# Kernel optimization log

Hardware: AMD Instinct MI355X
Metric: run time of the kernel (lower is better)

## Reference

```python
import jax, jax.numpy as jnp
import numpy as np

NUM_HEADS = 12
EPS = 1e-5


def _pool_norm(t, w, g, b, thw, stride):
    # t: [B, heads, 1+L, hd]. Depthwise Conv3d pooling on non-cls tokens, then LayerNorm(hd).
    B, Hn, _, hd = t.shape
    cls, body = t[:, :, :1], t[:, :, 1:]
    T, Hs, Ws = thw
    x = body.reshape(B * Hn, T, Hs, Ws, hd).transpose(0, 4, 1, 2, 3)  # [B*heads, hd, T, H, W]
    pad = [(w.shape[2] // 2,) * 2, (w.shape[3] // 2,) * 2, (w.shape[4] // 2,) * 2]
    y = jax.lax.conv_general_dilated(x, w, window_strides=stride, padding=pad,
                                     feature_group_count=hd,
                                     dimension_numbers=('NCDHW', 'OIDHW', 'NCDHW'))
    Tp, Hp, Wp = y.shape[2], y.shape[3], y.shape[4]
    y = y.reshape(B, Hn, hd, Tp * Hp * Wp).transpose(0, 1, 3, 2)  # [B, heads, Lp, hd]
    y = jnp.concatenate([cls, y], axis=2)
    mu = y.mean(-1, keepdims=True)
    var = ((y - mu) ** 2).mean(-1, keepdims=True)
    return (y - mu) * jax.lax.rsqrt(var + EPS) * g + b


def _forward(x, Wq, Wk, Wv, Wproj, b_proj, pq, pk, pv, gq, bq, gk, bk, gv, bv, thw):
    B, N, C = x.shape
    hd = C // NUM_HEADS
    def proj(W):
        return (x @ W.T).reshape(B, N, NUM_HEADS, hd).transpose(0, 2, 1, 3)  # [B, heads, N, hd]
    q = _pool_norm(proj(Wq), pq, gq, bq, thw, (1, 2, 2))
    k = _pool_norm(proj(Wk), pk, gk, bk, thw, (1, 4, 4))
    v = _pool_norm(proj(Wv), pv, gv, bv, thw, (1, 4, 4))
    scale = hd ** -0.5
    attn = jax.nn.softmax(jnp.einsum('bhqd,bhkd->bhqk', q * scale, k), axis=-1)
    o = jnp.einsum('bhqk,bhkd->bhqd', attn, v)
    o = o.transpose(0, 2, 1, 3).reshape(B, o.shape[2], C)
    return o @ Wproj.T + b_proj


def setup_inputs() -> dict:
    key = jax.random.key(0)
    ks = jax.random.split(key, 8)
    B, T, H, W, C = 8, 8, 28, 28, 768
    hd = C // NUM_HEADS
    N = T * H * W + 1  # cls token
    s = lambda k, sh: jax.random.normal(k, sh, jnp.float32) * 0.02
    return {
        'x': jax.random.normal(ks[0], (B, N, C), jnp.float32),
        'Wq': s(ks[1], (C, C)), 'Wk': s(ks[2], (C, C)), 'Wv': s(ks[3], (C, C)),
        'Wproj': s(ks[4], (C, C)), 'b_proj': jnp.zeros((C,), jnp.float32),
        'pool_q_w': s(ks[5], (hd, 1, 3, 3, 3)),
        'pool_k_w': s(ks[6], (hd, 1, 3, 3, 3)),
        'pool_v_w': s(ks[7], (hd, 1, 3, 3, 3)),
        'gq': jnp.ones((hd,), jnp.float32), 'bq': jnp.zeros((hd,), jnp.float32),
        'gk': jnp.ones((hd,), jnp.float32), 'bk': jnp.zeros((hd,), jnp.float32),
        'gv': jnp.ones((hd,), jnp.float32), 'bv': jnp.zeros((hd,), jnp.float32),
        'thw_t': 8, 'thw_h': 28, 'thw_w': 28,
    }


def reference(x, Wq, Wk, Wv, Wproj, b_proj, pool_q_w, pool_k_w, pool_v_w,
              gq, bq, gk, bk, gv, bv, thw_t, thw_h, thw_w):
    return _forward(x, Wq, Wk, Wv, Wproj, b_proj, pool_q_w, pool_k_w, pool_v_w,
                    gq, bq, gk, bk, gv, bv, (thw_t, thw_h, thw_w))
```

## Files before the change

### kernel.cpp

```cpp
#include <hip/hip_runtime.h>

using bf16   = __bf16;
using bf16x4 = __attribute__((ext_vector_type(4))) __bf16;
using bf16x8 = __attribute__((ext_vector_type(8))) __bf16;
using f32x4  = __attribute__((ext_vector_type(4))) float;
using u32x4  = __attribute__((ext_vector_type(4))) unsigned int;

#define MFMA16(a,b,c) __builtin_amdgcn_mfma_f32_16x16x32_bf16((a),(b),(c),0,0,0)

__device__ inline void glds16(const void* g, void* l) {
    __builtin_amdgcn_global_load_lds(
        (__attribute__((address_space(1))) void*)(const_cast<void*>(g)),
        (__attribute__((address_space(3))) void*)(l), 16, 0, 0);
}

__device__ inline int xcd_remap(int bid, int nwg) {
    const int xcd = bid & 7, loc = bid >> 3;
    const int q8 = nwg >> 3, r8 = nwg & 7;
    return (xcd < r8 ? xcd * (q8 + 1) : r8 * (q8 + 1) + (xcd - r8) * q8) + loc;
}

constexpr int CB   = 8;
constexpr int NH   = 12;
constexpr int CC   = 768;
constexpr int HD   = 64;
constexpr int TT   = 8, HH = 28, WW = 28;
constexpr int NTOK = TT*HH*WW + 1;
constexpr int MX   = CB*NTOK;
constexpr int MXP  = 50304;
constexpr int NQ   = 1569, NQP = 1600;
constexpr int NK   = 393,  NKP = 416;
constexpr int MO   = CB*NQ;
constexpr int MOP  = 12672;
constexpr int CTOK = 1 + TT*20*20;
constexpr int MKV  = CB*CTOK;
constexpr int MKVP = 25856;

__global__ __launch_bounds__(256) void cast_f32_bf16(const float* __restrict__ src,
                                                     bf16* __restrict__ dst,
                                                     int nvalid, int ntotal) {
    int i = (blockIdx.x * 256 + threadIdx.x) * 4;
    int stride = gridDim.x * 256 * 4;
    for (; i < ntotal; i += stride) {
        bf16x4 o;
        if (i + 3 < nvalid) {
            f32x4 v = *(const f32x4*)(src + i);
            #pragma unroll
            for (int e = 0; e < 4; ++e) o[e] = (bf16)v[e];
        } else {
            #pragma unroll
            for (int e = 0; e < 4; ++e) {
                int k = i + e;
                o[e] = (bf16)((k < nvalid) ? src[k] : 0.f);
            }
        }
        *(bf16x4*)(dst + i) = o;
    }
}

__global__ __launch_bounds__(256) void cast_w4(const float* __restrict__ w0,
                                               const float* __restrict__ w1,
                                               const float* __restrict__ w2,
                                               const float* __restrict__ w3,
                                               bf16* __restrict__ dst) {
    constexpr int WSZ = 589824;
    int i = (blockIdx.x * 256 + threadIdx.x) * 4;
    if (i >= 4 * WSZ) return;
    const int setn = i / WSZ, j = i % WSZ;
    const float* src = (setn == 0) ? w0 : (setn == 1) ? w1 : (setn == 2) ? w2 : w3;
    f32x4 v = *(const f32x4*)(src + j);
    bf16x4 o;
    #pragma unroll
    for (int e = 0; e < 4; ++e) o[e] = (bf16)v[e];
    *(bf16x4*)(dst + i) = o;
}

__global__ __launch_bounds__(256) void transpose_w3(const float* __restrict__ w0,
                                                    const float* __restrict__ w1,
                                                    const float* __restrict__ w2,
                                                    float* __restrict__ wt) {
    int i = blockIdx.x * 256 + threadIdx.x;
    if (i >= 3 * 1728) return;
    int setn = i / 1728, j = i % 1728;
    const float* src = (setn == 0) ? w0 : (setn == 1) ? w1 : w2;
    int tap = j / 64, c = j % 64;
    wt[i] = src[c * 27 + tap];
}

__global__ void bound_kernel(const float* __restrict__ gq, const float* __restrict__ bq,
                             const float* __restrict__ gk, const float* __restrict__ bk,
                             float* __restrict__ out) {
    const int c = threadIdx.x;
    float mgq = fabsf(gq[c]), sbq = bq[c] * bq[c];
    float mgk = fabsf(gk[c]), sbk = bk[c] * bk[c];
    #pragma unroll
    for (int m = 1; m < 64; m <<= 1) {
        mgq = fmaxf(mgq, __shfl_xor(mgq, m)); sbq += __shfl_xor(sbq, m);
        mgk = fmaxf(mgk, __shfl_xor(mgk, m)); sbk += __shfl_xor(sbk, m);
    }
    if (c == 0) {
        const float Bq = 8.f * mgq + sqrtf(sbq);
        const float Bk = 8.f * mgk + sqrtf(sbk);
        out[0] = 0.125f * Bq * Bk;
    }
}

__global__ __launch_bounds__(512, 2) void gemmU(const bf16* __restrict__ xb,
                                                const bf16* __restrict__ wqkv,
                                                bf16* __restrict__ tmpq,
                                                bf16* __restrict__ tmpkv) {
    extern __shared__ char lds[];
    const int wgid = xcd_remap(blockIdx.x, gridDim.x);

    const int tid = threadIdx.x, lane = tid & 63, w = tid >> 6;
    const int li = lane & 15, lg = lane >> 4;
    const int wr = w >> 2, wc = w & 3;
    const int lr  = lane >> 3;
    const int lsw = ((lane & 7) ^ lr) << 3;

    const bool isQ = wgid < 591;
    int bm, bn, Mv, ldc;
    const bf16* Bb;
    bf16* C;
    if (isQ) { bm = wgid / 3;        bn = wgid % 3;        Mv = MXP;  ldc = 768;
               Bb = wqkv + (size_t)bn * 256 * 768;               C = tmpq; }
    else     { int t = wgid - 591;   bm = t / 6; bn = t % 6; Mv = MKVP; ldc = 1536;
               Bb = wqkv + (size_t)(768 + bn * 256) * 768;       C = tmpkv; }

    const bf16* abase[4];
    const bf16* bbase[4];
    #pragma unroll
    for (int h_ = 0; h_ < 4; ++h_) {
        int gr = bm * 256 + h_ * 64 + w * 8 + lr;
        size_t orig;
        if (isQ) {
            if (gr > MXP - 1) gr = MXP - 1;
            orig = (size_t)gr;
        } else {
            if (gr > MKV - 1) gr = MKV - 1;
            const unsigned b = (unsigned)gr / 3201u;
            const unsigned p = (unsigned)gr % 3201u;
            if (p == 0) orig = (size_t)b * NTOK;
            else {
                const unsigned q  = p - 1;
                const unsigned t2 = q / 400u, rem = q % 400u;
                const unsigned hi = rem / 20u, wi = rem % 20u;
                const int ih = 4 * (int)((hi + 1) / 3) + (int)((hi + 1) % 3) - 1;
                const int iw = 4 * (int)((wi + 1) / 3) + (int)((wi + 1) % 3) - 1;
                orig = (size_t)b * NTOK + 1 + ((size_t)t2 * HH + ih) * WW + iw;
            }
        }
        abase[h_] = xb + orig * 768 + lsw;
        bbase[h_] = Bb + (size_t)(h_ * 64 + w * 8 + lr) * 768 + lsw;
    }

    const int sw_  = (li & 7) << 4;
    const int swc0 = (lg * 16) ^ sw_;
    const int swc1 = (64 | (lg * 16)) ^ sw_;

#define STAGE_T(Tt, buf) do {                                                        \
        char* d_ = lds + (buf) * 65536;                                              \
        _Pragma("unroll")                                                            \
        for (int h_ = 0; h_ < 4; ++h_)                                               \
            glds16(abase[h_] + (Tt) * 64, d_ + (h_ * 64 + w * 8) * 128);             \
        _Pragma("unroll")                                                            \
        for (int h_ = 0; h_ < 4; ++h_)                                               \
            glds16(bbase[h_] + (Tt) * 64, d_ + 32768 + (h_ * 64 + w * 8) * 128);     \
    } while (0)

    f32x4 acc[8][4] = {};
    bf16x8 aF[8], bF[4];

#define READ_K(sw)                                                                   \
    _Pragma("unroll") for (int mf = 0; mf < 8; ++mf)                                 \
        aF[mf] = *(const bf16x8*)(bufA + (size_t)(wr * 128 + mf * 16 + li) * 128 + (sw)); \
    _Pragma("unroll") for (int nf = 0; nf < 4; ++nf)                                 \
        bF[nf] = *(const bf16x8*)(bufB + (size_t)(wc * 64 + nf * 16 + li) * 128 + (sw));

#define MFMA_K()                                                                     \
    _Pragma("unroll") for (int mf = 0; mf < 8; ++mf)                                 \
    _Pragma("unroll") for (int nf = 0; nf < 4; ++nf)                                 \
        acc[mf][nf] = MFMA16(aF[mf], bF[nf], acc[mf][nf]);

    STAGE_T(0, 0);
    STAGE_T(1, 1);
    asm volatile("s_waitcnt vmcnt(8)" ::: "memory");
    __builtin_amdgcn_s_barrier();
    __builtin_amdgcn_sched_barrier(0);

    #pragma unroll
    for (int T = 0; T < 12; ++T) {
        const char* bufA = lds + (T & 1) * 65536;
        const char* bufB = bufA + 32768;
        if (T >= 1 && T < 11) STAGE_T(T + 1, (T + 1) & 1);
        READ_K(swc0);
        __builtin_amdgcn_s_setprio(1);
        MFMA_K();
        __builtin_amdgcn_s_setprio(0);
        READ_K(swc1);
        __builtin_amdgcn_s_setprio(1);
        MFMA_K();
        __builtin_amdgcn_s_setprio(0);
        asm volatile("s_waitcnt lgkmcnt(0)" ::: "memory");
        if (T < 11) asm volatile("s_waitcnt vmcnt(0)" ::: "memory");
        __builtin_amdgcn_s_barrier();
        __builtin_amdgcn_sched_barrier(0);
    }
#undef STAGE_T
#undef READ_K
#undef MFMA_K

    #pragma unroll
    for (int mf = 0; mf < 8; ++mf) {
        const int row0 = bm * 256 + wr * 128 + mf * 16 + lg * 4;
        #pragma unroll
        for (int nf = 0; nf < 4; ++nf) {
            const int col = bn * 256 + wc * 64 + nf * 16 + li;
            #pragma unroll
            for (int r = 0; r < 4; ++r) {
                const int row = row0 + r;
                if (row < Mv)
                    C[(size_t)row * ldc + col] = (bf16)acc[mf][nf][r];
            }
        }
    }
}

__global__ __launch_bounds__(512, 2) void gemmF(const bf16* __restrict__ A,
                                                const bf16* __restrict__ Bw,
                                                float* __restrict__ Cptr,
                                                const float* __restrict__ bias,
                                                int nbn, int Mvalid, int Aclamp) {
    extern __shared__ char lds[];
    const int wgid = xcd_remap(blockIdx.x, gridDim.x);
    const int bm = wgid / nbn, bn = wgid % nbn;

    const int tid = threadIdx.x, lane = tid & 63, w = tid >> 6;
    const int li = lane & 15, lg = lane >> 4;
    const int wr = w >> 2, wc = w & 3;
    const int lr  = lane >> 3;
    const int lsw = ((lane & 7) ^ lr) << 3;
    const bf16* Agp = A  + (size_t)bm * 256 * 768;
    const bf16* Bgp = Bw + (size_t)bn * 128 * 768;
    const int clampA = Aclamp - bm * 256;

    const int sw_  = (li & 7) << 4;
    const int swc0 = (lg * 16) ^ sw_;
    const int swc1 = (64 | (lg * 16)) ^ sw_;

#define STAGE_T(Tt, buf) do {                                                        \
        char* d_ = lds + (buf) * 49152;                                              \
        _Pragma("unroll")                                                            \
        for (int h_ = 0; h_ < 4; ++h_) {                                             \
            const int r0_ = h_ * 64 + w * 8;                                         \
            int gr_ = r0_ + lr; if (gr_ >= clampA) gr_ = clampA - 1;                 \
            glds16(Agp + (size_t)gr_ * 768 + (Tt) * 64 + lsw, d_ + r0_ * 128);       \
        }                                                                            \
        _Pragma("unroll")                                                            \
        for (int h_ = 0; h_ < 2; ++h_) {                                             \
            const int r0_ = h_ * 64 + w * 8;                                         \
            glds16(Bgp + (size_t)(r0_ + lr) * 768 + (Tt) * 64 + lsw,                 \
                   d_ + 32768 + r0_ * 128);                                          \
        } } while (0)

    f32x4 acc[8][2] = {};
    bf16x8 aF[8], bF[2];

#define READ_K(sw)                                                                   \
    _Pragma("unroll") for (int mf = 0; mf < 8; ++mf)                                 \
        aF[mf] = *(const bf16x8*)(bufA + (size_t)(wr * 128 + mf * 16 + li) * 128 + (sw)); \
    _Pragma("unroll") for (int nf = 0; nf < 2; ++nf)                                 \
        bF[nf] = *(const bf16x8*)(bufB + (size_t)(wc * 32 + nf * 16 + li) * 128 + (sw));

#define MFMA_K()                                                                     \
    _Pragma("unroll") for (int mf = 0; mf < 8; ++mf)                                 \
    _Pragma("unroll") for (int nf = 0; nf < 2; ++nf)                                 \
        acc[mf][nf] = MFMA16(aF[mf], bF[nf], acc[mf][nf]);

    STAGE_T(0, 0);
    STAGE_T(1, 1);
    asm volatile("s_waitcnt vmcnt(6)" ::: "memory");
    __builtin_amdgcn_s_barrier();
    __builtin_amdgcn_sched_barrier(0);

    #pragma unroll
    for (int T = 0; T < 12; ++T) {
        const char* bufA = lds + (T & 1) * 49152;
        const char* bufB = bufA + 32768;
        if (T >= 1 && T < 11) STAGE_T(T + 1, (T + 1) & 1);
        READ_K(swc0);
        __builtin_amdgcn_s_setprio(1);
        MFMA_K();
        __builtin_amdgcn_s_setprio(0);
        READ_K(swc1);
        __builtin_amdgcn_s_setprio(1);
        MFMA_K();
        __builtin_amdgcn_s_setprio(0);
        asm volatile("s_waitcnt lgkmcnt(0)" ::: "memory");
        if (T < 11) asm volatile("s_waitcnt vmcnt(0)" ::: "memory");
        __builtin_amdgcn_s_barrier();
        __builtin_amdgcn_sched_barrier(0);
    }
#undef STAGE_T
#undef READ_K
#undef MFMA_K

    #pragma unroll
    for (int mf = 0; mf < 8; ++mf) {
        const int row0 = bm * 256 + wr * 128 + mf * 16 + lg * 4;
        #pragma unroll
        for (int nf = 0; nf < 2; ++nf) {
            const int col = bn * 128 + wc * 32 + nf * 16 + li;
            #pragma unroll
            for (int r = 0; r < 4; ++r) {
                const int row = row0 + r;
                if (row < Mvalid)
                    Cptr[(size_t)row * 768 + col] = acc[mf][nf][r] + bias[col];
            }
        }
    }
}

template<int S, int OH, int OW, int CH, int NP, int NPpad, int SRCSTRIDE, bool COMPACT>
__global__ __launch_bounds__(256) void pool_norm2(const bf16* __restrict__ P,
                                                  const float* __restrict__ wt,
                                                  const float* __restrict__ gamma,
                                                  const float* __restrict__ beta,
                                                  bf16* __restrict__ outp,
                                                  float outScale) {
    constexpr int TASKS = TT * OH * CH + 1;
    const int w = threadIdx.x >> 6, lane = threadIdx.x & 63;
    const int gw = xcd_remap(blockIdx.x, gridDim.x) * 4 + w;
    const int bh = gw / TASKS, task = gw % TASKS;
    const int b = bh / NH, head = bh % NH;
    const int owg = lane >> 3, cg = lane & 7, c = cg * 8;
    const size_t rowbase = COMPACT ? (size_t)b * CTOK : (size_t)b * NTOK;
    const size_t pbase = rowbase * SRCSTRIDE + head * HD + c;

    if (task == TASKS - 1) {
        if (owg == 0) {
            bf16x8 v = *(const bf16x8*)(P + pbase);
            float a[8];
            #pragma unroll
            for (int e = 0; e < 8; ++e) a[e] = (float)v[e];
            float s = 0;
            #pragma unroll
            for (int e = 0; e < 8; ++e) s += a[e];
            s += __shfl_xor(s, 1); s += __shfl_xor(s, 2); s += __shfl_xor(s, 4);
            const float mu = s * 0.015625f;
            float v2 = 0;
            #pragma unroll
            for (int e = 0; e < 8; ++e) { float d = a[e] - mu; v2 += d * d; }
            v2 += __shfl_xor(v2, 1); v2 += __shfl_xor(v2, 2); v2 += __shfl_xor(v2, 4);
            const float rs = rsqrtf(v2 * 0.015625f + 1e-5f);
            f32x4 g0 = *(const f32x4*)(gamma + c), g1 = *(const f32x4*)(gamma + c + 4);
            f32x4 b0 = *(const f32x4*)(beta + c),  b1 = *(const f32x4*)(beta + c + 4);
            bf16x8 o;
            #pragma unroll
            for (int e = 0; e < 4; ++e) {
                o[e]     = (bf16)(((a[e]     - mu) * rs * g0[e] + b0[e]) * outScale);
                o[4 + e] = (bf16)(((a[4 + e] - mu) * rs * g1[e] + b1[e]) * outScale);
            }
            *(bf16x8*)(outp + ((size_t)bh * NPpad) * HD + c) = o;
        } else {
            bf16x8 z = {};
            for (int p = NP + owg - 1; p < NPpad; p += 7)
                *(bf16x8*)(outp + ((size_t)bh * NPpad + p) * HD + c) = z;
        }
        return;
    }

    const int t  = task / (OH * CH);
    const int r2 = task % (OH * CH);
    const int oh = r2 / CH;
    const int ow = (r2 % CH) * 8 + owg;
    const bool active = (ow < OW);

    float acc[8] = {0, 0, 0, 0, 0, 0, 0, 0};
    #pragma unroll
    for (int dt = 0; dt < 3; ++dt) {
        const int it = t + dt - 1;
        if (it < 0 || it >= TT) continue;
        #pragma unroll
        for (int dh = 0; dh < 3; ++dh) {
            int rowh;
            if constexpr (COMPACT) {
                const int hi = 3 * oh + dh - 1;
                if (hi < 0) continue;
                rowh = 1 + it * 400 + hi * 20;
            } else {
                const int ih = oh * S + dh - 1;
                if (ih < 0 || ih >= HH) continue;
                rowh = 1 + (it * HH + ih) * WW;
            }
            #pragma unroll
            for (int dw = 0; dw < 3; ++dw) {
                int rowoff;
                bool ok;
                if constexpr (COMPACT) {
                    const int wi = 3 * ow + dw - 1;
                    ok = active && (wi >= 0);
                    rowoff = rowh + wi;
                } else {
                    const int iw = ow * S + dw - 1;
                    ok = active && (iw >= 0);
                    rowoff = rowh + iw;
                }
                if (ok) {
                    bf16x8 v = *(const bf16x8*)(P + pbase + (size_t)rowoff * SRCSTRIDE);
                    const float* wp = wt + ((dt * 3 + dh) * 3 + dw) * 64 + c;
                    f32x4 w0 = *(const f32x4*)wp, w1 = *(const f32x4*)(wp + 4);
                    #pragma unroll
                    for (int e = 0; e < 4; ++e) {
                        acc[e]     += w0[e] * (float)v[e];
                        acc[4 + e] += w1[e] * (float)v[4 + e];
                    }
                }
            }
        }
    }
    float s = 0;
    #pragma unroll
    for (int e = 0; e < 8; ++e) s += acc[e];
    s += __shfl_xor(s, 1); s += __shfl_xor(s, 2); s += __shfl_xor(s, 4);
    const float mu = s * 0.015625f;
    float v2 = 0;
    #pragma unroll
    for (int e = 0; e < 8; ++e) { float d = acc[e] - mu; v2 += d * d; }
    v2 += __shfl_xor(v2, 1); v2 += __shfl_xor(v2, 2); v2 += __shfl_xor(v2, 4);
    const float rs = rsqrtf(v2 * 0.015625f + 1e-5f);
    if (active) {
        f32x4 g0 = *(const f32x4*)(gamma + c), g1 = *(const f32x4*)(gamma + c + 4);
        f32x4 b0 = *(const f32x4*)(beta + c),  b1 = *(const f32x4*)(beta + c + 4);
        bf16x8 o;
        #pragma unroll
        for (int e = 0; e < 4; ++e) {
            o[e]     = (bf16)(((acc[e]     - mu) * rs * g0[e] + b0[e]) * outScale);
            o[4 + e] = (bf16)(((acc[4 + e] - mu) * rs * g1[e] + b1[e]) * outScale);
        }
        const int p = 1 + (t * OH + oh) * OW + ow;
        *(bf16x8*)(outp + ((size_t)bh * NPpad + p) * HD + c) = o;
    }
}

__global__ __launch_bounds__(256) void attn_kernel(const bf16* __restrict__ qn,
                                                   const bf16* __restrict__ kn,
                                                   const bf16* __restrict__ vn,
                                                   bf16* __restrict__ ob,
                                                   const float* __restrict__ Mptr) {
    __shared__ bf16 Kl[2][32][72];
    __shared__ bf16 Vt[2][64][40];
    __shared__ bf16 Pl[4][16][40];

    const int tid = threadIdx.x, l = tid & 63, w = tid >> 6;
    const int li = l & 15, lg = l >> 4;
    const int wgid = xcd_remap(blockIdx.x, gridDim.x);
    const int bh = wgid / 25;
    const int b = bh / NH, head = bh % NH;
    const int qbase = (wgid % 25) * 64 + w * 16;
    const float M = Mptr[0];

    const bf16* qp = qn + ((size_t)bh * NQP + qbase + li) * HD + lg * 8;
    const bf16x8 aq0 = *(const bf16x8*)qp;
    const bf16x8 aq1 = *(const bf16x8*)(qp + 32);

    const int srow = tid >> 3, scol = (tid & 7) * 8;
    const int sj = tid & 31, sd8 = tid >> 5;
    const bf16* kbase = kn + (size_t)bh * NKP * HD;
    const bf16* vbase = vn + (size_t)bh * NKP * HD;

    u32x4 kv = *(const u32x4*)(kbase + srow * HD + scol);
    u32x4 vv = *(const u32x4*)(vbase + sj * HD + sd8 * 8);
    *(u32x4*)&Kl[0][srow][scol] = kv;
    {
        bf16x8 t = __builtin_bit_cast(bf16x8, vv);
        #pragma unroll
        for (int e = 0; e < 8; ++e) Vt[0][sd8 * 8 + e][sj] = t[e];
    }

    f32x4 oacc[4] = {};
    float lpart[4] = {0.f, 0.f, 0.f, 0.f};

    for (int kt = 0; kt < 13; ++kt) {
        const int cur = kt & 1;
        if (kt < 12) {
            kv = *(const u32x4*)(kbase + (kt + 1) * 32 * HD + srow * HD + scol);
            vv = *(const u32x4*)(vbase + (kt + 1) * 32 * HD + sj * HD + sd8 * 8);
        }
        __syncthreads();

        f32x4 c0 = {}, c1 = {};
        const bf16x8 b00 = *(const bf16x8*)&Kl[cur][li][lg * 8];
        const bf16x8 b01 = *(const bf16x8*)&Kl[cur][li][32 + lg * 8];
        const bf16x8 b10 = *(const bf16x8*)&Kl[cur][16 + li][lg * 8];
        const bf16x8 b11 = *(const bf16x8*)&Kl[cur][16 + li][32 + lg * 8];
        __builtin_amdgcn_s_setprio(1);
        c0 = MFMA16(aq0, b00, c0); c0 = MFMA16(aq1, b01, c0);
        c1 = MFMA16(aq0, b10, c1); c1 = MFMA16(aq1, b11, c1);
        __builtin_amdgcn_s_setprio(0);

        float p0[4], p1[4];
        #pragma unroll
        for (int r = 0; r < 4; ++r) {
            p0[r] = __expf(c0[r] - M);
            p1[r] = __expf(c1[r] - M);
        }
        if (kt == 12) {
            const bool m0 = (384 + li) >= NK;
            #pragma unroll
            for (int r = 0; r < 4; ++r) { if (m0) p0[r] = 0.f; p1[r] = 0.f; }
        }
        #pragma unroll
        for (int r = 0; r < 4; ++r) {
            lpart[r] += p0[r] + p1[r];
            Pl[w][lg * 4 + r][li]      = (bf16)p0[r];
            Pl[w][lg * 4 + r][16 + li] = (bf16)p1[r];
        }
        const bf16x8 ap = *(const bf16x8*)&Pl[w][li][lg * 8];
        __builtin_amdgcn_s_setprio(1);
        #pragma unroll
        for (int dg = 0; dg < 4; ++dg) {
            const bf16x8 bv = *(const bf16x8*)&Vt[cur][dg * 16 + li][lg * 8];
            oacc[dg] = MFMA16(ap, bv, oacc[dg]);
        }
        __builtin_amdgcn_s_setprio(0);

        if (kt < 12) {
            const int nxt = cur ^ 1;
            *(u32x4*)&Kl[nxt][srow][scol] = kv;
            bf16x8 t = __builtin_bit_cast(bf16x8, vv);
            #pragma unroll
            for (int e = 0; e < 8; ++e) Vt[nxt][sd8 * 8 + e][sj] = t[e];
        }
    }
    #pragma unroll
    for (int r = 0; r < 4; ++r) {
        float lsum = lpart[r];
        lsum += __shfl_xor(lsum, 1);
        lsum += __shfl_xor(lsum, 2);
        lsum += __shfl_xor(lsum, 4);
        lsum += __shfl_xor(lsum, 8);
        const int q = qbase + lg * 4 + r;
        if (q < NQ) {
            const float inv = 1.f / lsum;
            const size_t off = ((size_t)(b * NQ + q)) * CC + head * HD;
            #pragma unroll
            for (int dg = 0; dg < 4; ++dg)
                ob[off + dg * 16 + li] = (bf16)(oacc[dg][r] * inv);
        }
    }
}

extern "C" void kernel_launch(void* const* d_in, const int* in_sizes, int n_in,
                              void* d_out, int out_size, void* d_ws, size_t ws_size,
                              hipStream_t stream) {
    const float* x     = (const float*)d_in[0];
    const float* Wq    = (const float*)d_in[1];
    const float* Wk    = (const float*)d_in[2];
    const float* Wv    = (const float*)d_in[3];
    const float* Wproj = (const float*)d_in[4];
    const float* bproj = (const float*)d_in[5];
    const float* pqw   = (const float*)d_in[6];
    const float* pkw   = (const float*)d_in[7];
    const float* pvw   = (const float*)d_in[8];
    const float* gq    = (const float*)d_in[9];
    const float* bq    = (const float*)d_in[10];
    const float* gk    = (const float*)d_in[11];
    const float* bk    = (const float*)d_in[12];
    const float* gv    = (const float*)d_in[13];
    const float* bv    = (const float*)d_in[14];

    if (ws_size < 364000000ULL) return;
    char* ws = (char*)d_ws;
    bf16* xb    = (bf16*)(ws);
    bf16* wqkv  = (bf16*)(ws + 77266944);
    bf16* wpb   = (bf16*)(ws + 80805888);
    bf16* tmpq  = (bf16*)(ws + 81985536);
    bf16* tmpkv = (bf16*)(ws + 159252480);
    bf16* qn    = (bf16*)(ws + 238682112);
    bf16* kn    = (bf16*)(ws + 258342912);
    bf16* vnb   = (bf16*)(ws + 263454720);
    bf16* ob    = (bf16*)(ws + 268566528);
    float* wt   = (float*)(ws + 288030720);
    float* Mb   = (float*)(ws + 288051456);

    (void)hipFuncSetAttribute((const void*)gemmU,
                              hipFuncAttributeMaxDynamicSharedMemorySize, 131072);
    (void)hipFuncSetAttribute((const void*)gemmF,
                              hipFuncAttributeMaxDynamicSharedMemorySize, 98304);

    transpose_w3<<<21, 256, 0, stream>>>(pqw, pkw, pvw, wt);
    bound_kernel<<<1, 64, 0, stream>>>(gq, bq, gk, bk, Mb);
    cast_f32_bf16<<<4096, 256, 0, stream>>>(x, xb, MX * CC, MXP * CC);
    cast_w4<<<2304, 256, 0, stream>>>(Wq, Wk, Wv, Wproj, wqkv);

    gemmU<<<1197, 512, 131072, stream>>>(xb, wqkv, tmpq, tmpkv);

    pool_norm2<2, 14, 14, 2, NQ, NQP, 768,  false><<<5400, 256, 0, stream>>>(tmpq,        wt,        gq, bq, qn,  0.125f);
    pool_norm2<4, 7, 7, 1, NK, NKP, 1536, true ><<<1368, 256, 0, stream>>>(tmpkv,       wt + 1728, gk, bk, kn,  1.0f);
    pool_norm2<4, 7, 7, 1, NK, NKP, 1536, true ><<<1368, 256, 0, stream>>>(tmpkv + 768, wt + 3456, gv, bv, vnb, 1.0f);

    attn_kernel<<<2400, 256, 0, stream>>>(qn, kn, vnb, ob, Mb);

    gemmF<<<50 * 6, 512, 98304, stream>>>(ob, wpb, (float*)d_out, bproj, 6, MO, MOP);
}
```

Before: 352.9 us.

## Split GEMM K-loop into four quadrant phases with interleaved half-tile prefetch

```diff
diff --git a/kernel.cpp b/kernel.cpp
--- a/kernel.cpp
+++ b/kernel.cpp
@@ -158,57 +158,82 @@
     const int swc0 = (lg * 16) ^ sw_;
     const int swc1 = (64 | (lg * 16)) ^ sw_;
 
-#define STAGE_T(Tt, buf) do {                                                        \
-        char* d_ = lds + (buf) * 65536;                                              \
-        _Pragma("unroll")                                                            \
-        for (int h_ = 0; h_ < 4; ++h_)                                               \
-            glds16(abase[h_] + (Tt) * 64, d_ + (h_ * 64 + w * 8) * 128);             \
-        _Pragma("unroll")                                                            \
-        for (int h_ = 0; h_ < 4; ++h_)                                               \
-            glds16(bbase[h_] + (Tt) * 64, d_ + 32768 + (h_ * 64 + w * 8) * 128);     \
+#define STAGE_AH(Tt, a) do {                                                         \
+        char* d_ = lds + ((Tt) & 1) * 65536;                                         \
+        glds16(abase[2*(a)]   + (size_t)(Tt) * 64, d_ + ((2*(a))   * 64 + w * 8) * 128); \
+        glds16(abase[2*(a)+1] + (size_t)(Tt) * 64, d_ + ((2*(a)+1) * 64 + w * 8) * 128); \
     } while (0)
+#define STAGE_BH(Tt, b) do {                                                         \
+        char* d_ = lds + ((Tt) & 1) * 65536 + 32768;                                 \
+        glds16(bbase[2*(b)]   + (size_t)(Tt) * 64, d_ + ((2*(b))   * 64 + w * 8) * 128); \
+        glds16(bbase[2*(b)+1] + (size_t)(Tt) * 64, d_ + ((2*(b)+1) * 64 + w * 8) * 128); \
+    } while (0)
 
     f32x4 acc[8][4] = {};
-    bf16x8 aF[8], bF[4];
-
-#define READ_K(sw)                                                                   \
-    _Pragma("unroll") for (int mf = 0; mf < 8; ++mf)                                 \
-        aF[mf] = *(const bf16x8*)(bufA + (size_t)(wr * 128 + mf * 16 + li) * 128 + (sw)); \
-    _Pragma("unroll") for (int nf = 0; nf < 4; ++nf)                                 \
-        bF[nf] = *(const bf16x8*)(bufB + (size_t)(wc * 64 + nf * 16 + li) * 128 + (sw));
-
-#define MFMA_K()                                                                     \
-    _Pragma("unroll") for (int mf = 0; mf < 8; ++mf)                                 \
-    _Pragma("unroll") for (int nf = 0; nf < 4; ++nf)                                 \
-        acc[mf][nf] = MFMA16(aF[mf], bF[nf], acc[mf][nf]);
-
-    STAGE_T(0, 0);
-    STAGE_T(1, 1);
-    asm volatile("s_waitcnt vmcnt(8)" ::: "memory");
+    bf16x8 aF[4][2], bF0[2][2], bF1[2][2];
+
+#define READ_A(mh)                                                                   \
+    _Pragma("unroll") for (int mf = 0; mf < 4; ++mf) {                               \
+        const char* p_ = bufA + (size_t)(wr * 128 + (mh) * 64 + mf * 16 + li) * 128; \
+        aF[mf][0] = *(const bf16x8*)(p_ + swc0);                                     \
+        aF[mf][1] = *(const bf16x8*)(p_ + swc1); }
+#define READ_B(nh, BF)                                                               \
+    _Pragma("unroll") for (int nf = 0; nf < 2; ++nf) {                               \
+        const char* p_ = bufB + (size_t)(wc * 64 + (nh) * 32 + nf * 16 + li) * 128;  \
+        BF[nf][0] = *(const bf16x8*)(p_ + swc0);                                     \
+        BF[nf][1] = *(const bf16x8*)(p_ + swc1); }
+#define MFMA_PH(mh, nh, BF)                                                          \
+    _Pragma("unroll") for (int mf = 0; mf < 4; ++mf)                                 \
+    _Pragma("unroll") for (int nf = 0; nf < 2; ++nf) {                               \
+        acc[(mh)*4+mf][(nh)*2+nf] = MFMA16(aF[mf][0], BF[nf][0], acc[(mh)*4+mf][(nh)*2+nf]); \
+        acc[(mh)*4+mf][(nh)*2+nf] = MFMA16(aF[mf][1], BF[nf][1], acc[(mh)*4+mf][(nh)*2+nf]); }
+
+    STAGE_BH(0, 0); STAGE_BH(0, 1); STAGE_AH(0, 0); STAGE_AH(0, 1);
+    STAGE_BH(1, 0); STAGE_BH(1, 1); STAGE_AH(1, 0);
+    asm volatile("s_waitcnt vmcnt(6)" ::: "memory");
     __builtin_amdgcn_s_barrier();
-    __builtin_amdgcn_sched_barrier(0);
-
-    #pragma unroll
-    for (int T = 0; T < 12; ++T) {
-        const char* bufA = lds + (T & 1) * 65536;
+
+    #pragma unroll
+    for (int k = 0; k < 12; ++k) {
+        const char* bufA = lds + (k & 1) * 65536;
         const char* bufB = bufA + 32768;
-        if (T >= 1 && T < 11) STAGE_T(T + 1, (T + 1) & 1);
-        READ_K(swc0);
-        __builtin_amdgcn_s_setprio(1);
-        MFMA_K();
-        __builtin_amdgcn_s_setprio(0);
-        READ_K(swc1);
-        __builtin_amdgcn_s_setprio(1);
-        MFMA_K();
-        __builtin_amdgcn_s_setprio(0);
+        READ_A(0); READ_B(0, bF0);
+        if (k < 11) STAGE_AH(k + 1, 1);
+        __builtin_amdgcn_s_barrier();
         asm volatile("s_waitcnt lgkmcnt(0)" ::: "memory");
-        if (T < 11) asm volatile("s_waitcnt vmcnt(0)" ::: "memory");
-        __builtin_amdgcn_s_barrier();
-        __builtin_amdgcn_sched_barrier(0);
-    }
-#undef STAGE_T
-#undef READ_K
-#undef MFMA_K
+        __builtin_amdgcn_s_setprio(1);
+        MFMA_PH(0, 0, bF0);
+        __builtin_amdgcn_s_setprio(0);
+        __builtin_amdgcn_s_barrier();
+        READ_B(1, bF1);
+        __builtin_amdgcn_s_barrier();
+        asm volatile("s_waitcnt lgkmcnt(0)" ::: "memory");
+        __builtin_amdgcn_s_setprio(1);
+        MFMA_PH(0, 1, bF1);
+        __builtin_amdgcn_s_setprio(0);
+        __builtin_amdgcn_s_barrier();
+        READ_A(1);
+        if (k < 10) { STAGE_BH(k + 2, 0); STAGE_BH(k + 2, 1); }
+        __builtin_amdgcn_s_barrier();
+        asm volatile("s_waitcnt lgkmcnt(0)" ::: "memory");
+        __builtin_amdgcn_s_setprio(1);
+        MFMA_PH(1, 0, bF0);
+        __builtin_amdgcn_s_setprio(0);
+        __builtin_amdgcn_s_barrier();
+        if (k < 10) STAGE_AH(k + 2, 0);
+        __builtin_amdgcn_s_barrier();
+        __builtin_amdgcn_s_setprio(1);
+        MFMA_PH(1, 1, bF1);
+        __builtin_amdgcn_s_setprio(0);
+        if (k < 10)       asm volatile("s_waitcnt vmcnt(6)" ::: "memory");
+        else if (k == 10) asm volatile("s_waitcnt vmcnt(0)" ::: "memory");
+        __builtin_amdgcn_s_barrier();
+    }
+#undef STAGE_AH
+#undef STAGE_BH
+#undef READ_A
+#undef READ_B
+#undef MFMA_PH
 
     #pragma unroll
     for (int mf = 0; mf < 8; ++mf) {
```

After: 349.6 us. Within noise of the previous version (-0.9%).
